# Performance work log

Hardware: AMD Instinct MI355X
Metric: run time of the kernel (lower is better)

The kernel has to match this reference:

```python
import jax, jax.numpy as jnp
import numpy as np

DIM = 384
HEADS = 12
WH, WW = 7, 7
N = WH * WW
HEAD_DIM = DIM // HEADS
SCALE = HEAD_DIM ** -0.5


def _double_step_seq(step1, len1, step2, len2):
    seq1 = np.arange(0, step1 * len1, step1)
    seq2 = np.arange(0, step2 * len2, step2)
    return (seq1[:, None] + seq2[None, :]).reshape(1, -1)


def _rel_position_index():
    coords = _double_step_seq(2 * WW - 1, WH, 1, WW)  # (1, N)
    idx = coords + coords.T                            # (N, N)
    idx = idx[:, ::-1].copy()                          # flip along dim 1
    return jnp.asarray(idx, dtype=jnp.int32)

REL_IDX = _rel_position_index()


def setup_inputs() -> dict:
    key = jax.random.key(0)
    ks = jax.random.split(key, 6)
    B_ = 4096
    x = jax.random.normal(ks[0], (B_, N, DIM), dtype=jnp.float32)
    mask = jnp.zeros((64, N, N), dtype=jnp.float32)
    qkv_w = jax.random.normal(ks[1], (3 * DIM, DIM), dtype=jnp.float32) * 0.02
    qkv_b = jax.random.normal(ks[2], (3 * DIM,), dtype=jnp.float32) * 0.02
    proj_w = jax.random.normal(ks[3], (DIM, DIM), dtype=jnp.float32) * 0.02
    proj_b = jax.random.normal(ks[4], (DIM,), dtype=jnp.float32) * 0.02
    bias_table = jax.random.normal(ks[5], (169, HEADS), dtype=jnp.float32) * 0.02
    return {"x": x, "mask": mask, "qkv_w": qkv_w, "qkv_b": qkv_b,
            "proj_w": proj_w, "proj_b": proj_b, "bias_table": bias_table}


def reference(x, mask, qkv_w, qkv_b, proj_w, proj_b, bias_table):
    B_, n, C = x.shape
    # qkv projection: (B_, N, 3C) -> (3, B_, H, N, d)
    qkv = (x @ qkv_w.T + qkv_b).reshape(B_, n, 3, HEADS, HEAD_DIM)
    qkv = jnp.transpose(qkv, (2, 0, 3, 1, 4))
    q, k, v = qkv[0], qkv[1], qkv[2]
    q = q * SCALE
    attn = jnp.einsum('bhnd,bhmd->bhnm', q, k)  # (B_, H, N, N)
    # gathered relative position bias: (H, N, N)
    rel_bias = bias_table[REL_IDX.reshape(-1)].reshape(n, n, HEADS)
    rel_bias = jnp.transpose(rel_bias, (2, 0, 1))
    attn = attn + rel_bias[None]
    nW = mask.shape[0]
    attn = attn.reshape(B_ // nW, nW, HEADS, n, n) + mask[None, :, None]
    attn = attn.reshape(B_, HEADS, n, n)
    attn = jax.nn.softmax(attn, axis=-1)
    out = jnp.einsum('bhnm,bhmd->bnhd', attn, v).reshape(B_, n, C)
    out = out @ proj_w.T + proj_b
    return out
```

## Files before the change

kernel.cpp:

```cpp
#include <hip/hip_runtime.h>
#include <hip/hip_bf16.h>

#define NTOK 49
#define DIMC 384
#define NH 12
#define QSCALE 0.17677669529663687f

typedef __attribute__((ext_vector_type(8))) short short8;
typedef __attribute__((ext_vector_type(4))) float f32x4;
typedef unsigned int u32;

#define WQB2_SHORTS (54 * 8192)
#define WPB_SHORTS  (18 * 8192)

__device__ __forceinline__ short f2bf(float f) {
    __bf16 h = (__bf16)f;
    return __builtin_bit_cast(short, h);
}
__device__ __forceinline__ float bf2f(short s) {
    u32 u = ((u32)(unsigned short)s) << 16;
    return __builtin_bit_cast(float, u);
}
__device__ __forceinline__ int cof(int p) { return 13 * (p / 7) + (p % 7); }

__device__ __forceinline__ void gld_lds16(const void* g, void* l) {
    __builtin_amdgcn_global_load_lds(
        (const __attribute__((address_space(1))) u32*)g,
        (__attribute__((address_space(3))) u32*)l, 16, 0, 0);
}

__device__ __forceinline__ short8 gather_bf(const float* __restrict__ w, int row, int k0) {
    const float* p = w + row * DIMC + k0;
    float4 a = *(const float4*)p;
    float4 b = *(const float4*)(p + 4);
    short8 r;
    r[0]=f2bf(a.x); r[1]=f2bf(a.y); r[2]=f2bf(a.z); r[3]=f2bf(a.w);
    r[4]=f2bf(b.x); r[5]=f2bf(b.y); r[6]=f2bf(b.z); r[7]=f2bf(b.w);
    return r;
}

__global__ void prep2(const float* __restrict__ qw, const float* __restrict__ pw,
                      short* __restrict__ wqb2, short* __restrict__ wpb) {
    int gt = blockIdx.x * 256 + threadIdx.x;
    int tile = gt >> 10;
    int rem = gt & 1023;
    int r = rem >> 3, g = rem & 7;
    int kc = tile % 6;
    int k0 = kc * 64 + ((g ^ (r & 7)) << 3);
    short8 o;
    if (tile < 54) {
        int nb = tile / 6;
        const float* src = qw + (size_t)(nb * 128 + r) * DIMC + k0;
        #pragma unroll
        for (int e = 0; e < 8; ++e) o[e] = f2bf(src[e]);
        *(short8*)(wqb2 + (size_t)tile * 8192 + r * 64 + g * 8) = o;
    } else {
        int t2 = tile - 54;
        int nb = t2 / 6;
        const float* src = pw + (size_t)(nb * 128 + r) * DIMC + k0;
        #pragma unroll
        for (int e = 0; e < 8; ++e) o[e] = f2bf(src[e]);
        *(short8*)(wpb + (size_t)t2 * 8192 + r * 64 + g * 8) = o;
    }
}

__global__ __launch_bounds__(1024)
void prep_x(const float* __restrict__ x, short* __restrict__ xa, int w0) {
    const int bid = blockIdx.x;
    const int mt = bid / 6, kc = bid % 6;
    const int tid = threadIdx.x;
    const int r = tid >> 3, g = tid & 7;
    const int win = w0 + mt * 2 + (r >> 6);
    const int tok = r & 63;
    const int k0 = kc * 64 + ((g ^ (r & 7)) << 3);
    short8 o;
    if (tok < NTOK) {
        const float* src = x + ((size_t)win * NTOK + tok) * DIMC + k0;
        float4 a = *(const float4*)src;
        float4 b = *(const float4*)(src + 4);
        o[0]=f2bf(a.x); o[1]=f2bf(a.y); o[2]=f2bf(a.z); o[3]=f2bf(a.w);
        o[4]=f2bf(b.x); o[5]=f2bf(b.y); o[6]=f2bf(b.z); o[7]=f2bf(b.w);
    } else {
        o = (short8)0;
    }
    *(short8*)(xa + ((size_t)mt * 6 + kc) * 8192 + r * 64 + g * 8) = o;
}

__global__ __launch_bounds__(256, 2)
void qkv_gemm(const short* __restrict__ xa, const float* __restrict__ qkv_b,
              const short* __restrict__ wqb2, short* __restrict__ qkvb)
{
    __shared__ char LC[2][32768] __attribute__((aligned(128)));

    const int tid = threadIdx.x;
    const int wv = tid >> 6, lane = tid & 63;
    const int l15 = lane & 15, l4 = lane >> 4;
    const int wr = wv >> 1, wc = wv & 1;
    const int sg = blockIdx.x / 72, bb = blockIdx.x % 72;
    const int mb = sg * 8 + (bb & 7), nb = bb >> 3;

    const char* asrc = (const char*)xa + (size_t)mb * 6 * 16384;
    const char* bsrc = (const char*)wqb2 + (size_t)(nb * 6) * 8192 * 2;

    f32x4 acc[4][4];
    #pragma unroll
    for (int mi = 0; mi < 4; ++mi)
        #pragma unroll
        for (int ni = 0; ni < 4; ++ni) acc[mi][ni] = (f32x4){0.f, 0.f, 0.f, 0.f};

    #pragma unroll
    for (int it = 0; it < 4; ++it) {
        int L = (wv * 4 + it) * 1024;
        gld_lds16(asrc + L + lane * 16, &LC[0][L]);
        gld_lds16(bsrc + L + lane * 16, &LC[0][16384 + L]);
    }

    #pragma unroll
    for (int kc = 0; kc < 6; ++kc) {
        __builtin_amdgcn_sched_barrier(0);
        asm volatile("s_waitcnt vmcnt(0)" ::: "memory");
        __builtin_amdgcn_s_barrier();
        __builtin_amdgcn_sched_barrier(0);
        if (kc < 5) {
            #pragma unroll
            for (int it = 0; it < 4; ++it) {
                int L = (wv * 4 + it) * 1024;
                gld_lds16(asrc + (kc + 1) * 16384 + L + lane * 16, &LC[(kc + 1) & 1][L]);
                gld_lds16(bsrc + (kc + 1) * 16384 + L + lane * 16, &LC[(kc + 1) & 1][16384 + L]);
            }
        }
        const char* bufp = LC[kc & 1];
        __builtin_amdgcn_s_setprio(1);
        #pragma unroll
        for (int ksub = 0; ksub < 2; ++ksub) {
            short8 a[4], b[4];
            #pragma unroll
            for (int mi = 0; mi < 4; ++mi) {
                int row = wr * 64 + mi * 16 + l15;
                a[mi] = *(const short8*)(bufp + row * 128 +
                        ((ksub * 64 + l4 * 16) ^ ((row & 7) << 4)));
            }
            #pragma unroll
            for (int ni = 0; ni < 4; ++ni) {
                int row = wc * 64 + ni * 16 + l15;
                b[ni] = *(const short8*)(bufp + 16384 + row * 128 +
                        ((ksub * 64 + l4 * 16) ^ ((row & 7) << 4)));
            }
            #pragma unroll
            for (int mi = 0; mi < 4; ++mi)
                #pragma unroll
                for (int ni = 0; ni < 4; ++ni)
                    acc[mi][ni] = __builtin_amdgcn_mfma_f32_16x16x32_bf16(
                        a[mi], b[ni], acc[mi][ni], 0, 0, 0);
        }
        __builtin_amdgcn_s_setprio(0);
    }

    __syncthreads();

    float bias[4];
    #pragma unroll
    for (int ni = 0; ni < 4; ++ni) bias[ni] = qkv_b[nb * 128 + wc * 64 + ni * 16 + l15];

    char* slab = (char*)LC + wv * 8192;
    const int wl = mb * 2 + wr;
    const int sub = nb / 3;

    if (sub < 2) {
        #pragma unroll
        for (int mi = 0; mi < 4; ++mi)
            #pragma unroll
            for (int ni = 0; ni < 4; ++ni)
                #pragma unroll
                for (int reg = 0; reg < 4; ++reg) {
                    float v = acc[mi][ni][reg] + bias[ni];
                    if (sub == 0) v *= QSCALE;
                    int rowp = mi * 16 + l4 * 4 + reg, colp = ni * 16 + l15;
                    *(short*)(slab + rowp * 128 + ((colp * 2) ^ ((rowp & 7) << 4))) = f2bf(v);
                }
        __builtin_amdgcn_sched_barrier(0);
        asm volatile("s_waitcnt lgkmcnt(0)" ::: "memory");
        __builtin_amdgcn_sched_barrier(0);
        #pragma unroll
        for (int hh = 0; hh < 2; ++hh)
            #pragma unroll
            for (int s = 0; s < 4; ++s) {
                int head = (nb % 3) * 4 + wc * 2 + hh;
                int rowp = s * 16 + l15;
                short8 frag = *(const short8*)(slab + rowp * 128 +
                              ((hh * 64 + l4 * 16) ^ ((rowp & 7) << 4)));
                *(short8*)(qkvb + (((size_t)wl * NH + head) * 12 + sub * 4 + s) * 512 + lane * 8) = frag;
            }
    } else {
        #pragma unroll
        for (int mi = 0; mi < 4; ++mi)
            #pragma unroll
            for (int ni = 0; ni < 4; ++ni)
                #pragma unroll
                for (int reg = 0; reg < 4; ++reg) {
                    float v = acc[mi][ni][reg] + bias[ni];
                    int rowp = mi * 16 + l4 * 4 + reg, colp = ni * 16 + l15;
                    *(short*)(slab + colp * 128 + ((rowp * 2) ^ ((colp & 7) << 4))) = f2bf(v);
                }
        __builtin_amdgcn_sched_barrier(0);
        asm volatile("s_waitcnt lgkmcnt(0)" ::: "memory");
        __builtin_amdgcn_sched_barrier(0);
        #pragma unroll
        for (int hh = 0; hh < 2; ++hh)
            #pragma unroll
            for (int dt = 0; dt < 2; ++dt)
                #pragma unroll
                for (int kst = 0; kst < 2; ++kst) {
                    int head = (nb - 6) * 4 + wc * 2 + hh;
                    int row2 = hh * 32 + dt * 16 + l15;
                    short8 frag = *(const short8*)(slab + row2 * 128 +
                                  ((kst * 64 + l4 * 16) ^ ((row2 & 7) << 4)));
                    *(short8*)(qkvb + (((size_t)wl * NH + head) * 12 + 8 + dt * 2 + kst) * 512 + lane * 8) = frag;
                }
    }
}

#define AVS_OFF 0
#define BB_OFF  49152
#define PS_OFF2 49152
#define BT_OFF2 57344
#define APL_TOT 81920

__global__ __launch_bounds__(256)
void attnproj(const float* __restrict__ mask, const float* __restrict__ bias_table,
              const short* __restrict__ qkvb, const short* __restrict__ wpb,
              const float* __restrict__ proj_b, float* __restrict__ out, int w0)
{
    __shared__ char SB[APL_TOT] __attribute__((aligned(128)));
    short* BT = (short*)(SB + BT_OFF2);

    const int tid = threadIdx.x;
    const int wv = tid >> 6, lane = tid & 63;
    const int l15 = lane & 15, l4 = lane >> 4;
    const int st4 = wv;
    const int lw = blockIdx.x;
    const int win = w0 + lw;

    for (int i = tid; i < 169 * NH; i += 256) BT[i] = f2bf(bias_table[i]);

    u32 mvp[4][2];
    int bidx[4][4];
    {
        const float* maskp = mask + (size_t)(win & 63) * (NTOK * NTOK);
        #pragma unroll
        for (int t = 0; t < 4; ++t) {
            int m = t * 16 + l15;
            float pad = (m < NTOK) ? 0.f : -1e30f;
            #pragma unroll
            for (int rp = 0; rp < 2; ++rp) {
                float v[2];
                #pragma unroll
                for (int e = 0; e < 2; ++e) {
                    int i = st4 * 16 + l4 * 4 + rp * 2 + e;
                    v[e] = ((i < NTOK && m < NTOK) ? maskp[i * NTOK + m] : 0.f) + pad;
                }
                mvp[t][rp] = (u32)(unsigned short)f2bf(v[0]) |
                             ((u32)(unsigned short)f2bf(v[1]) << 16);
            }
        }
        int cofi[4], cofm[4];
        #pragma unroll
        for (int t = 0; t < 4; ++t) {
            int m = t * 16 + l15;
            cofm[t] = cof(48 - (m < NTOK ? m : 48));
        }
        #pragma unroll
        for (int reg = 0; reg < 4; ++reg) {
            int i = st4 * 16 + l4 * 4 + reg;
            cofi[reg] = cof(i < NTOK ? i : 48);
        }
        #pragma unroll
        for (int t = 0; t < 4; ++t)
            #pragma unroll
            for (int reg = 0; reg < 4; ++reg)
                bidx[t][reg] = (cofi[reg] + cofm[t]) * NH;
    }
    const f32x4 zf = (f32x4){0.f, 0.f, 0.f, 0.f};
    __syncthreads();

    const short* qh = qkvb + (size_t)lw * (NH * 12 * 512);
    char* psw = SB + PS_OFF2 + wv * 2048;

    #pragma unroll 1
    for (int h = 0; h < NH; ++h) {
        const short* hb = qh + h * (12 * 512) + lane * 8;
        short8 q = *(const short8*)(hb + st4 * 512);
        short8 kf[4], vf[4];
        #pragma unroll
        for (int t = 0; t < 4; ++t) kf[t] = *(const short8*)(hb + (4 + t) * 512);
        #pragma unroll
        for (int j = 0; j < 4; ++j) vf[j] = *(const short8*)(hb + (8 + j) * 512);

        f32x4 sc[4];
        #pragma unroll
        for (int t = 0; t < 4; ++t)
            sc[t] = __builtin_amdgcn_mfma_f32_16x16x32_bf16(q, kf[t], zf, 0, 0, 0);

        float p[4][4];
        #pragma unroll
        for (int t = 0; t < 4; ++t)
            #pragma unroll
            for (int reg = 0; reg < 4; ++reg) {
                u32 pk = mvp[t][reg >> 1];
                float mval = bf2f((short)((reg & 1) ? (pk >> 16) : (pk & 0xffff)));
                float bt = bf2f(BT[bidx[t][reg] + h]);
                p[t][reg] = sc[t][reg] + mval + bt;
            }
        #pragma unroll
        for (int reg = 0; reg < 4; ++reg) {
            float mx = fmaxf(fmaxf(p[0][reg], p[1][reg]), fmaxf(p[2][reg], p[3][reg]));
            #pragma unroll
            for (int off = 8; off >= 1; off >>= 1) mx = fmaxf(mx, __shfl_xor(mx, off, 64));
            float s0 = 0.f;
            #pragma unroll
            for (int t = 0; t < 4; ++t) { p[t][reg] = __expf(p[t][reg] - mx); s0 += p[t][reg]; }
            #pragma unroll
            for (int off = 8; off >= 1; off >>= 1) s0 += __shfl_xor(s0, off, 64);
            float rs = 1.f / s0;
            #pragma unroll
            for (int t = 0; t < 4; ++t) p[t][reg] *= rs;
        }
        #pragma unroll
        for (int t = 0; t < 4; ++t)
            #pragma unroll
            for (int reg = 0; reg < 4; ++reg) {
                int r = l4 * 4 + reg;
                int byt = r * 128 + ((((t * 16 + l15) << 1)) ^ ((r & 7) << 4));
                *(short*)(psw + byt) = f2bf(p[t][reg]);
            }
        f32x4 av[2];
        av[0] = zf; av[1] = zf;
        #pragma unroll
        for (int kst = 0; kst < 2; ++kst) {
            short8 pa;
            {
                int byt = l15 * 128 + (((kst * 64 + l4 * 16)) ^ ((l15 & 7) << 4));
                pa = *(const short8*)(psw + byt);
            }
            #pragma unroll
            for (int dt = 0; dt < 2; ++dt)
                av[dt] = __builtin_amdgcn_mfma_f32_16x16x32_bf16(pa, vf[dt * 2 + kst], av[dt], 0, 0, 0);
        }
        #pragma unroll
        for (int dt = 0; dt < 2; ++dt)
            #pragma unroll
            for (int reg = 0; reg < 4; ++reg) {
                int tok = st4 * 16 + l4 * 4 + reg;
                if (tok < NTOK) {
                    int lb = (h * 32 + dt * 16 + l15) * 2;
                    *(short*)(SB + AVS_OFF + tok * 768 + (lb ^ ((tok & 7) << 4))) = f2bf(av[dt][reg]);
                }
            }
    }

    asm volatile("s_waitcnt lgkmcnt(0)" ::: "memory");
    __builtin_amdgcn_s_barrier();
    __builtin_amdgcn_sched_barrier(0);

    const char* bsrc = (const char*)wpb;
    char* BB = SB + BB_OFF;

    #pragma unroll
    for (int it = 0; it < 4; ++it) {
        int L = it * 4096 + wv * 1024;
        gld_lds16(bsrc + L + lane * 16, BB + L);
    }

    f32x4 acc[4][2];
    #pragma unroll
    for (int mi = 0; mi < 4; ++mi) { acc[mi][0] = zf; acc[mi][1] = zf; }

    #pragma unroll 1
    for (int t = 0; t < 18; ++t) {
        const int kc = t % 6, nb = t / 6;
        __builtin_amdgcn_sched_barrier(0);
        asm volatile("s_waitcnt vmcnt(0)" ::: "memory");
        __builtin_amdgcn_s_barrier();
        __builtin_amdgcn_sched_barrier(0);
        if (t < 17) {
            #pragma unroll
            for (int it = 0; it < 4; ++it) {
                int L = it * 4096 + wv * 1024;
                gld_lds16(bsrc + (size_t)(t + 1) * 16384 + L + lane * 16,
                          BB + ((t + 1) & 1) * 16384 + L);
            }
        }
        const char* bufp = BB + (t & 1) * 16384;
        __builtin_amdgcn_s_setprio(1);
        #pragma unroll
        for (int ksub = 0; ksub < 2; ++ksub) {
            short8 a[4], b[2];
            #pragma unroll
            for (int mi = 0; mi < 4; ++mi) {
                int row = mi * 16 + l15;
                a[mi] = *(const short8*)(SB + AVS_OFF + row * 768 +
                        ((kc * 128 + ksub * 64 + l4 * 16) ^ ((row & 7) << 4)));
            }
            #pragma unroll
            for (int ni = 0; ni < 2; ++ni) {
                int row = st4 * 32 + ni * 16 + l15;
                b[ni] = *(const short8*)(bufp + row * 128 +
                        ((ksub * 64 + l4 * 16) ^ ((row & 7) << 4)));
            }
            #pragma unroll
            for (int mi = 0; mi < 4; ++mi)
                #pragma unroll
                for (int ni = 0; ni < 2; ++ni)
                    acc[mi][ni] = __builtin_amdgcn_mfma_f32_16x16x32_bf16(
                        a[mi], b[ni], acc[mi][ni], 0, 0, 0);
        }
        __builtin_amdgcn_s_setprio(0);
        if (kc == 5) {
            #pragma unroll
            for (int ni = 0; ni < 2; ++ni) {
                const int col = nb * 128 + st4 * 32 + ni * 16 + l15;
                const float pb = proj_b[col];
                #pragma unroll
                for (int mi = 0; mi < 4; ++mi)
                    #pragma unroll
                    for (int reg = 0; reg < 4; ++reg) {
                        int tok = mi * 16 + l4 * 4 + reg;
                        if (tok < NTOK)
                            out[((size_t)win * NTOK + tok) * DIMC + col] = acc[mi][ni][reg] + pb;
                    }
            }
            #pragma unroll
            for (int mi = 0; mi < 4; ++mi) { acc[mi][0] = zf; acc[mi][1] = zf; }
        }
    }
}

__global__ __launch_bounds__(256, 2)
void winattn_fallback(const float* __restrict__ x, const float* __restrict__ mask,
                      const float* __restrict__ qkv_w, const float* __restrict__ qkv_b,
                      const float* __restrict__ proj_w, const float* __restrict__ proj_b,
                      const float* __restrict__ bias_table, float* __restrict__ out)
{
    __shared__ short SL[26624] __attribute__((aligned(128)));
    const int tid = threadIdx.x, wv = tid >> 6, lane = tid & 63;
    const int l15 = lane & 15, l4 = lane >> 4;
    const int win = blockIdx.x;
    const int xbase = win * (NTOK * DIMC);
    const int KSo = 0, VTo = 2048, PSo = 4096, QAo = 8192;

    short8 xf[12];
    {
        const int row = wv * 16 + l15;
        const bool valid = row < NTOK;
        const float* xr = x + xbase + row * DIMC;
        #pragma unroll
        for (int ks = 0; ks < 12; ++ks)
            xf[ks] = valid ? gather_bf(xr, 0, ks * 32 + l4 * 8) : (short8)0;
    }
    float mv[4][4]; int bidx[4][4];
    {
        const float* maskp = mask + (win & 63) * (NTOK * NTOK);
        int cofi[4], cofm[4];
        float negm[4];
        #pragma unroll
        for (int t = 0; t < 4; ++t) {
            int m = t * 16 + l15;
            negm[t] = (m < NTOK) ? 0.f : -1e30f;
            cofm[t] = cof(48 - (m < NTOK ? m : 48));
            #pragma unroll
            for (int reg = 0; reg < 4; ++reg) {
                int i = wv * 16 + l4 * 4 + reg;
                mv[t][reg] = ((i < NTOK && m < NTOK) ? maskp[i * NTOK + m] : 0.f) + negm[t];
            }
        }
        #pragma unroll
        for (int reg = 0; reg < 4; ++reg) {
            int i = wv * 16 + l4 * 4 + reg;
            cofi[reg] = cof(i < NTOK ? i : 48);
        }
        #pragma unroll
        for (int t = 0; t < 4; ++t)
            #pragma unroll
            for (int reg = 0; reg < 4; ++reg) bidx[t][reg] = (cofi[reg] + cofm[t]) * NH;
    }
    f32x4 pacc[24];
    #pragma unroll
    for (int t = 0; t < 24; ++t) pacc[t] = (f32x4){0.f, 0.f, 0.f, 0.f};
    const f32x4 zf = (f32x4){0.f, 0.f, 0.f, 0.f};
    __syncthreads();

    #pragma unroll 1
    for (int h = 0; h < NH; ++h) {
        f32x4 qa[6];
        #pragma unroll
        for (int nt = 0; nt < 6; ++nt) qa[nt] = zf;
        #pragma unroll
        for (int nt = 0; nt < 6; ++nt) {
            const int grow = (nt >> 1) * DIMC + h * 32 + (nt & 1) * 16 + l15;
            #pragma unroll
            for (int ks = 0; ks < 12; ++ks) {
                short8 b = gather_bf(qkv_w, grow, ks * 32 + l4 * 8);
                qa[nt] = __builtin_amdgcn_mfma_f32_16x16x32_bf16(xf[ks], b, qa[nt], 0, 0, 0);
            }
        }
        #pragma unroll
        for (int nt = 0; nt < 6; ++nt) {
            const int sub = nt >> 1;
            const int colw = (nt & 1) * 16 + l15;
            const float bias = qkv_b[sub * DIMC + h * 32 + colw];
            #pragma unroll
            for (int reg = 0; reg < 4; ++reg) {
                const int tokg = wv * 16 + l4 * 4 + reg;
                float val = qa[nt][reg] + bias;
                if (sub == 0) {
                    int byt = tokg * 64 + ((colw << 1) ^ ((tokg & 3) << 4));
                    SL[QAo + (byt >> 1)] = f2bf(val * QSCALE);
                } else if (sub == 1) {
                    int byt = tokg * 64 + ((colw << 1) ^ ((tokg & 3) << 4));
                    SL[KSo + (byt >> 1)] = f2bf(val);
                } else {
                    int byt = colw * 128 + ((tokg << 1) ^ ((colw & 7) << 4));
                    SL[VTo + (byt >> 1)] = f2bf(val);
                }
            }
        }
        __syncthreads();
        short8 aq;
        { int row = wv*16+l15; int byt = row*64 + ((l4*16) ^ ((row&3)<<4));
          aq = *(const short8*)&SL[QAo + (byt>>1)]; }
        f32x4 sc[4];
        #pragma unroll
        for (int t = 0; t < 4; ++t) {
            int row = t*16+l15; int byt = row*64 + ((l4*16) ^ ((row&3)<<4));
            short8 bk = *(const short8*)&SL[KSo + (byt>>1)];
            sc[t] = __builtin_amdgcn_mfma_f32_16x16x32_bf16(aq, bk, zf, 0, 0, 0);
        }
        float p[4][4];
        #pragma unroll
        for (int t = 0; t < 4; ++t)
            #pragma unroll
            for (int reg = 0; reg < 4; ++reg)
                p[t][reg] = sc[t][reg] + mv[t][reg] + bias_table[bidx[t][reg] + h];
        #pragma unroll
        for (int reg = 0; reg < 4; ++reg) {
            float mx = fmaxf(fmaxf(p[0][reg], p[1][reg]), fmaxf(p[2][reg], p[3][reg]));
            #pragma unroll
            for (int off = 8; off >= 1; off >>= 1) mx = fmaxf(mx, __shfl_xor(mx, off, 64));
            float s0 = 0.f;
            #pragma unroll
            for (int t = 0; t < 4; ++t) { p[t][reg] = __expf(p[t][reg] - mx); s0 += p[t][reg]; }
            #pragma unroll
            for (int off = 8; off >= 1; off >>= 1) s0 += __shfl_xor(s0, off, 64);
            float rs = 1.f / s0;
            #pragma unroll
            for (int t = 0; t < 4; ++t) p[t][reg] *= rs;
        }
        #pragma unroll
        for (int t = 0; t < 4; ++t)
            #pragma unroll
            for (int reg = 0; reg < 4; ++reg) {
                int row = wv*16 + l4*4 + reg;
                int byt = row*128 + (((t*16+l15) << 1) ^ ((row&7)<<4));
                SL[PSo + (byt>>1)] = f2bf(p[t][reg]);
            }
        f32x4 av[2]; av[0] = zf; av[1] = zf;
        #pragma unroll
        for (int kst = 0; kst < 2; ++kst) {
            short8 pa;
            { int row = wv*16+l15; int byt = row*128 + ((kst*64+l4*16) ^ ((row&7)<<4));
              pa = *(const short8*)&SL[PSo + (byt>>1)]; }
            #pragma unroll
            for (int dt = 0; dt < 2; ++dt) {
                int d = dt*16+l15; int byt = d*128 + ((kst*64+l4*16) ^ ((d&7)<<4));
                short8 bv = *(const short8*)&SL[VTo + (byt>>1)];
                av[dt] = __builtin_amdgcn_mfma_f32_16x16x32_bf16(pa, bv, av[dt], 0, 0, 0);
            }
        }
        __syncthreads();
        #pragma unroll
        for (int dt = 0; dt < 2; ++dt)
            #pragma unroll
            for (int reg = 0; reg < 4; ++reg) {
                int row = wv*16 + l4*4 + reg;
                int byt = row*64 + (((dt*16+l15) << 1) ^ ((row&3)<<4));
                SL[QAo + (byt>>1)] = f2bf(av[dt][reg]);
            }
        __syncthreads();
        short8 aa;
        { int row = wv*16+l15; int byt = row*64 + ((l4*16) ^ ((row&3)<<4));
          aa = *(const short8*)&SL[QAo + (byt>>1)]; }
        #pragma unroll
        for (int nt = 0; nt < 24; ++nt) {
            short8 bp = gather_bf(proj_w, nt * 16 + l15, h * 32 + l4 * 8);
            pacc[nt] = __builtin_amdgcn_mfma_f32_16x16x32_bf16(aa, bp, pacc[nt], 0, 0, 0);
        }
    }
    {
        float* op = out + xbase;
        #pragma unroll
        for (int nt = 0; nt < 24; ++nt) {
            const float pb = proj_b[nt * 16 + l15];
            #pragma unroll
            for (int reg = 0; reg < 4; ++reg) {
                const int i = wv * 16 + l4 * 4 + reg;
                if (i < NTOK) op[i * DIMC + nt * 16 + l15] = pacc[nt][reg] + pb;
            }
        }
    }
}

extern "C" void kernel_launch(void* const* d_in, const int* in_sizes, int n_in,
                              void* d_out, int out_size, void* d_ws, size_t ws_size,
                              hipStream_t stream) {
    const float* x          = (const float*)d_in[0];
    const float* mask       = (const float*)d_in[1];
    const float* qkv_w      = (const float*)d_in[2];
    const float* qkv_b      = (const float*)d_in[3];
    const float* proj_w     = (const float*)d_in[4];
    const float* proj_b     = (const float*)d_in[5];
    const float* bias_table = (const float*)d_in[6];
    float* out = (float*)d_out;

    const size_t fixed = ((size_t)WQB2_SHORTS + WPB_SHORTS) * 2;
    auto need = [&](int c) {
        size_t wpc = 4096 / c;
        size_t mbc = wpc / 2;
        return fixed + mbc * 98304UL  + wpc * 147456UL ;
    };
    int c = 0;
    if (ws_size >= need(4)) c = 4;
    else if (ws_size >= need(8)) c = 8;
    else if (ws_size >= need(16)) c = 16;

    if (c) {
        short* wqb2 = (short*)d_ws;
        short* wpb  = wqb2 + WQB2_SHORTS;
        const int wpc = 4096 / c;
        const int mbc = wpc / 2;
        short* xa   = wpb + WPB_SHORTS;
        short* qkvb = xa + (size_t)mbc * 49152;

        prep2<<<288, 256, 0, stream>>>(qkv_w, proj_w, wqb2, wpb);
        for (int ch = 0; ch < c; ++ch) {
            const int w0 = ch * wpc;
            prep_x<<<mbc * 6, 1024, 0, stream>>>(x, xa, w0);
            qkv_gemm<<<mbc * 9, 256, 0, stream>>>(xa, qkv_b, wqb2, qkvb);
            attnproj<<<wpc, 256, 0, stream>>>(mask, bias_table, qkvb, wpb, proj_b, out, w0);
        }
    } else {
        winattn_fallback<<<4096, 256, 0, stream>>>(x, mask, qkv_w, qkv_b, proj_w,
                                                   proj_b, bias_table, out);
    }
}
```

Before: 767.4 us.

## Load QKV GEMM A operand directly into registers, halve LDS, raise occupancy

The QKV GEMM now stages only the weight (B) tiles through double-buffered LDS. Each wave reads its activation (A) fragments straight from global memory into registers, using precomputed swizzled offsets, and prefetches the next k-chunk after the MFMAs. This halves LDS use per block, which lets the launch bound request three blocks per CU instead of two. In exchange, the A loads are no longer shared through LDS, so the two column-waves fetch the same data redundantly. Their latency is also only partly hidden, because the prefetch is issued after compute and waited on at the next barrier.

```diff
diff --git a/kernel.cpp b/kernel.cpp
--- a/kernel.cpp
+++ b/kernel.cpp
@@ -86,11 +86,11 @@
     *(short8*)(xa + ((size_t)mt * 6 + kc) * 8192 + r * 64 + g * 8) = o;
 }
 
-__global__ __launch_bounds__(256, 2)
+__global__ __launch_bounds__(256, 3)
 void qkv_gemm(const short* __restrict__ xa, const float* __restrict__ qkv_b,
               const short* __restrict__ wqb2, short* __restrict__ qkvb)
 {
-    __shared__ char LC[2][32768] __attribute__((aligned(128)));
+    __shared__ char LB[2][16384] __attribute__((aligned(128)));
 
     const int tid = threadIdx.x;
     const int wv = tid >> 6, lane = tid & 63;
@@ -100,7 +100,16 @@
     const int mb = sg * 8 + (bb & 7), nb = bb >> 3;
 
     const char* asrc = (const char*)xa + (size_t)mb * 6 * 16384;
-    const char* bsrc = (const char*)wqb2 + (size_t)(nb * 6) * 8192 * 2;
+    const char* bsrc = (const char*)wqb2 + (size_t)(nb * 6) * 16384;
+
+    int aoff[8];
+    #pragma unroll
+    for (int ksub = 0; ksub < 2; ++ksub)
+        #pragma unroll
+        for (int mi = 0; mi < 4; ++mi) {
+            int row = wr * 64 + mi * 16 + l15;
+            aoff[ksub * 4 + mi] = row * 128 + ((ksub * 64 + l4 * 16) ^ ((row & 7) << 4));
+        }
 
     f32x4 acc[4][4];
     #pragma unroll
@@ -108,12 +117,14 @@
         #pragma unroll
         for (int ni = 0; ni < 4; ++ni) acc[mi][ni] = (f32x4){0.f, 0.f, 0.f, 0.f};
 
+    short8 af[8];
     #pragma unroll
     for (int it = 0; it < 4; ++it) {
-        int L = (wv * 4 + it) * 1024;
-        gld_lds16(asrc + L + lane * 16, &LC[0][L]);
-        gld_lds16(bsrc + L + lane * 16, &LC[0][16384 + L]);
-    }
+        int L = it * 4096 + wv * 1024;
+        gld_lds16(bsrc + L + lane * 16, &LB[0][0] + L);
+    }
+    #pragma unroll
+    for (int f = 0; f < 8; ++f) af[f] = *(const short8*)(asrc + aoff[f]);
 
     #pragma unroll
     for (int kc = 0; kc < 6; ++kc) {
@@ -124,26 +135,20 @@
         if (kc < 5) {
             #pragma unroll
             for (int it = 0; it < 4; ++it) {
-                int L = (wv * 4 + it) * 1024;
-                gld_lds16(asrc + (kc + 1) * 16384 + L + lane * 16, &LC[(kc + 1) & 1][L]);
-                gld_lds16(bsrc + (kc + 1) * 16384 + L + lane * 16, &LC[(kc + 1) & 1][16384 + L]);
-            }
-        }
-        const char* bufp = LC[kc & 1];
+                int L = it * 4096 + wv * 1024;
+                gld_lds16(bsrc + (kc + 1) * 16384 + L + lane * 16,
+                          &LB[(kc + 1) & 1][0] + L);
+            }
+        }
+        const char* bufp = LB[kc & 1];
         __builtin_amdgcn_s_setprio(1);
         #pragma unroll
         for (int ksub = 0; ksub < 2; ++ksub) {
-            short8 a[4], b[4];
-            #pragma unroll
-            for (int mi = 0; mi < 4; ++mi) {
-                int row = wr * 64 + mi * 16 + l15;
-                a[mi] = *(const short8*)(bufp + row * 128 +
-                        ((ksub * 64 + l4 * 16) ^ ((row & 7) << 4)));
-            }
+            short8 b[4];
             #pragma unroll
             for (int ni = 0; ni < 4; ++ni) {
                 int row = wc * 64 + ni * 16 + l15;
-                b[ni] = *(const short8*)(bufp + 16384 + row * 128 +
+                b[ni] = *(const short8*)(bufp + row * 128 +
                         ((ksub * 64 + l4 * 16) ^ ((row & 7) << 4)));
             }
             #pragma unroll
@@ -151,9 +156,15 @@
                 #pragma unroll
                 for (int ni = 0; ni < 4; ++ni)
                     acc[mi][ni] = __builtin_amdgcn_mfma_f32_16x16x32_bf16(
-                        a[mi], b[ni], acc[mi][ni], 0, 0, 0);
+                        af[ksub * 4 + mi], b[ni], acc[mi][ni], 0, 0, 0);
         }
         __builtin_amdgcn_s_setprio(0);
+        __builtin_amdgcn_sched_barrier(0);
+        if (kc < 5) {
+            #pragma unroll
+            for (int f = 0; f < 8; ++f)
+                af[f] = *(const short8*)(asrc + (kc + 1) * 16384 + aoff[f]);
+        }
     }
 
     __syncthreads();
@@ -162,7 +173,7 @@
     #pragma unroll
     for (int ni = 0; ni < 4; ++ni) bias[ni] = qkv_b[nb * 128 + wc * 64 + ni * 16 + l15];
 
-    char* slab = (char*)LC + wv * 8192;
+    char* slab = (char*)LB + wv * 8192;
     const int wl = mb * 2 + wr;
     const int sub = nb / 3;
 
```

Result: no change. 774.8 us (+1.0%).
